# Performance work log

Hardware: AMD Instinct MI355X
Metric: run time of the kernel (lower is better)

## Reference

```python
import jax, jax.numpy as jnp
import numpy as np

E = 1024

def setup_inputs() -> dict:
    key = jax.random.key(0)
    ks = jax.random.split(key, 9)
    s = 1.0 / np.sqrt(E)
    return {
        "x": jax.random.normal(ks[0], (4, 2048, E), dtype=jnp.float32),
        "Wq": jax.random.uniform(ks[1], (E, E), jnp.float32, -s, s),
        "bq": jax.random.uniform(ks[2], (E,), jnp.float32, -s, s),
        "Wk": jax.random.uniform(ks[3], (E, E), jnp.float32, -s, s),
        "bk": jax.random.uniform(ks[4], (E,), jnp.float32, -s, s),
        "Wv": jax.random.uniform(ks[5], (E, E), jnp.float32, -s, s),
        "bv": jax.random.uniform(ks[6], (E,), jnp.float32, -s, s),
        "Wo": jax.random.uniform(ks[7], (E, E), jnp.float32, -s, s),
        "bo": jax.random.uniform(ks[8], (E,), jnp.float32, -s, s),
    }

def reference(x, Wq, bq, Wk, bk, Wv, bv, Wo, bo):
    # Note: the torch module never splits heads; attention is over full embed_dim.
    # nn.Linear: y = x @ W.T + b
    Q = jnp.einsum('bse,fe->bsf', x, Wq) + bq
    K = jnp.einsum('bse,fe->bsf', x, Wk) + bk
    V = jnp.einsum('bse,fe->bsf', x, Wv) + bv
    scale = 1.0 / jnp.sqrt(jnp.asarray(x.shape[-1], x.dtype))
    scores = jnp.einsum('bqe,bke->bqk', Q, K) * scale  # [B, S, S]
    weights = jax.nn.softmax(scores, axis=-1)
    out = jnp.einsum('bqk,bke->bqe', weights, V)
    # dropout is identity in eval mode
    return jnp.einsum('bse,fe->bsf', out, Wo) + bo
```

## Files before the change

kernel.cpp:

```cpp
#include <hip/hip_runtime.h>
#include <hip/hip_bf16.h>
#include <stdint.h>

typedef short bf16x8 __attribute__((ext_vector_type(8)));
typedef float f32x4 __attribute__((ext_vector_type(4)));
typedef __attribute__((address_space(3))) void lds_void_t;
typedef __attribute__((address_space(1))) void g_void_t;

static __device__ __forceinline__ unsigned short f2b(float f) {
    __hip_bfloat16 b = __float2bfloat16(f);
    return __builtin_bit_cast(unsigned short, b);
}
static __device__ __forceinline__ float b2f(unsigned int u) {
    return __builtin_bit_cast(float, u << 16);
}

__global__ __launch_bounds__(256) void cast_f32_bf16(
    const float* __restrict__ in, ushort* __restrict__ out, int n4)
{
    int i = blockIdx.x * blockDim.x + threadIdx.x;
    const int stride = gridDim.x * blockDim.x;
    for (; i < n4; i += stride) {
        float4 v = reinterpret_cast<const float4*>(in)[i];
        ushort4 o;
        o.x = f2b(v.x); o.y = f2b(v.y); o.z = f2b(v.z); o.w = f2b(v.w);
        reinterpret_cast<ushort4*>(out)[i] = o;
    }
}

__global__ __launch_bounds__(256) void concat_bias(
    const float* __restrict__ b0, const float* __restrict__ b1,
    const float* __restrict__ b2, float* __restrict__ out)
{
    const int i = blockIdx.x * blockDim.x + threadIdx.x;
    const int sec = i >> 10, off = i & 1023;
    out[i] = sec == 0 ? b0[off] : (sec == 1 ? b1[off] : b2[off]);
}

template<typename CT, bool HAS_BIAS>
__global__ __launch_bounds__(256, 4)
void gemm_bt(const ushort* __restrict__ A, const ushort* __restrict__ B,
             const float* __restrict__ bias, CT* __restrict__ C,
             int lda, int ldb, int ldc, int K,
             long strideA, long strideB, long strideC, float alpha)
{
    __shared__ __align__(16) ushort sA[128 * 64];
    __shared__ __align__(16) ushort sB[128 * 64];

    const int bz = blockIdx.z;
    A += (size_t)bz * strideA;
    B += (size_t)bz * strideB;
    C += (size_t)bz * strideC;

    const int gx = gridDim.x, gy = gridDim.y;
    const int nwg = gx * gy;
    int bx = blockIdx.x, by = blockIdx.y;
    if ((nwg & 7) == 0) {
        const int flat = blockIdx.x + gx * blockIdx.y;
        const int cpx = nwg >> 3;
        const int u = (flat & 7) * cpx + (flat >> 3);
        bx = u % gx;
        by = u / gx;
    }

    const int tid = threadIdx.x;
    const int w   = tid >> 6;
    const int l   = tid & 63;
    const int wr  = w >> 1;
    const int wc  = w & 1;

    const int bRow = by * 128;
    const int bCol = bx * 128;

    const int lr   = l >> 3;
    const int scol = (((l & 7) ^ lr) << 3);

    f32x4 acc[4][4];
#pragma unroll
    for (int m = 0; m < 4; ++m)
#pragma unroll
        for (int n = 0; n < 4; ++n)
            acc[m][n] = f32x4{0.f, 0.f, 0.f, 0.f};

    for (int k0 = 0; k0 < K; k0 += 64) {
#pragma unroll
        for (int p = 0; p < 4; ++p) {
            const int c   = p * 4 + w;
            const int row = c * 8 + lr;
            const ushort* gA = A + (size_t)(bRow + row) * lda + (k0 + scol);
            const ushort* gB = B + (size_t)(bCol + row) * ldb + (k0 + scol);
            __builtin_amdgcn_global_load_lds((const g_void_t*)gA,
                (lds_void_t*)((char*)sA + c * 1024), 16, 0, 0);
            __builtin_amdgcn_global_load_lds((const g_void_t*)gB,
                (lds_void_t*)((char*)sB + c * 1024), 16, 0, 0);
        }
        __syncthreads();

        bf16x8 af[4][2], bfv[4][2];
#pragma unroll
        for (int m = 0; m < 4; ++m) {
            const int ar = wr * 64 + m * 16 + (l & 15);
#pragma unroll
            for (int ks = 0; ks < 2; ++ks) {
                const int slot = (ks * 4 + (l >> 4)) ^ (ar & 7);
                af[m][ks] = *reinterpret_cast<const bf16x8*>(
                    (const char*)sA + ar * 128 + slot * 16);
            }
        }
#pragma unroll
        for (int n = 0; n < 4; ++n) {
            const int br = wc * 64 + n * 16 + (l & 15);
#pragma unroll
            for (int ks = 0; ks < 2; ++ks) {
                const int slot = (ks * 4 + (l >> 4)) ^ (br & 7);
                bfv[n][ks] = *reinterpret_cast<const bf16x8*>(
                    (const char*)sB + br * 128 + slot * 16);
            }
        }
#pragma unroll
        for (int ks = 0; ks < 2; ++ks)
#pragma unroll
            for (int m = 0; m < 4; ++m)
#pragma unroll
                for (int n = 0; n < 4; ++n)
                    acc[m][n] = __builtin_amdgcn_mfma_f32_16x16x32_bf16(
                        af[m][ks], bfv[n][ks], acc[m][n], 0, 0, 0);
        __syncthreads();
    }

    const int cl = l & 15;
#pragma unroll
    for (int n = 0; n < 4; ++n) {
        const int col = bCol + wc * 64 + n * 16 + cl;
        const float bv = HAS_BIAS ? bias[col] : 0.f;
#pragma unroll
        for (int m = 0; m < 4; ++m) {
#pragma unroll
            for (int r = 0; r < 4; ++r) {
                const int row = bRow + wr * 64 + m * 16 + (l >> 4) * 4 + r;
                const float v = (acc[m][n][r] + bv) * alpha;
                if constexpr (sizeof(CT) == 2)
                    ((ushort*)C)[(size_t)row * ldc + col] = f2b(v);
                else
                    ((float*)C)[(size_t)row * ldc + col] = v;
            }
        }
    }
}

__global__ __launch_bounds__(256) void softmax_rows(ushort* __restrict__ S)
{
    __shared__ float red[8];
    const size_t row = blockIdx.x;
    ushort* p = S + row * 2048;
    const int tid = threadIdx.x;

    uint4 v = reinterpret_cast<uint4*>(p)[tid];
    float f[8];
    const unsigned int* wv = reinterpret_cast<const unsigned int*>(&v);
#pragma unroll
    for (int j = 0; j < 4; ++j) {
        f[2 * j]     = b2f(wv[j] & 0xFFFFu);
        f[2 * j + 1] = b2f(wv[j] >> 16);
    }
    float mx = f[0];
#pragma unroll
    for (int j = 1; j < 8; ++j) mx = fmaxf(mx, f[j]);
#pragma unroll
    for (int s = 1; s < 64; s <<= 1) mx = fmaxf(mx, __shfl_xor(mx, s));
    if ((tid & 63) == 0) red[tid >> 6] = mx;
    __syncthreads();
    mx = fmaxf(fmaxf(red[0], red[1]), fmaxf(red[2], red[3]));

    float sum = 0.f;
#pragma unroll
    for (int j = 0; j < 8; ++j) { f[j] = __expf(f[j] - mx); sum += f[j]; }
#pragma unroll
    for (int s = 1; s < 64; s <<= 1) sum += __shfl_xor(sum, s);
    if ((tid & 63) == 0) red[4 + (tid >> 6)] = sum;
    __syncthreads();
    sum = (red[4] + red[5]) + (red[6] + red[7]);
    const float inv = 1.0f / sum;

    uint4 o;
    unsigned int* wo = reinterpret_cast<unsigned int*>(&o);
#pragma unroll
    for (int j = 0; j < 4; ++j) {
        const unsigned int lo = f2b(f[2 * j] * inv);
        const unsigned int hi = f2b(f[2 * j + 1] * inv);
        wo[j] = lo | (hi << 16);
    }
    reinterpret_cast<uint4*>(p)[tid] = o;
}

__global__ __launch_bounds__(256) void transpose_v(
    const ushort* __restrict__ V, ushort* __restrict__ Vt, int ldv, long strideV)
{
    __shared__ ushort t[64][65];
    const int b  = blockIdx.z;
    const int e0 = blockIdx.x * 64;
    const int s0 = blockIdx.y * 64;
    const int tid = threadIdx.x;
    const int cg = (tid & 15) * 4;
    const int r0 = tid >> 4;

    const ushort* Vb = V + (size_t)b * strideV;
#pragma unroll
    for (int p = 0; p < 4; ++p) {
        const int r = r0 + p * 16;
        ushort4 x = *reinterpret_cast<const ushort4*>(
            Vb + (size_t)(s0 + r) * ldv + e0 + cg);
        t[r][cg + 0] = x.x; t[r][cg + 1] = x.y;
        t[r][cg + 2] = x.z; t[r][cg + 3] = x.w;
    }
    __syncthreads();
    ushort* Vtb = Vt + (size_t)b * 1024 * 2048;
#pragma unroll
    for (int p = 0; p < 4; ++p) {
        const int e = r0 + p * 16;
        ushort4 o;
        o.x = t[cg + 0][e]; o.y = t[cg + 1][e];
        o.z = t[cg + 2][e]; o.w = t[cg + 3][e];
        *reinterpret_cast<ushort4*>(Vtb + (size_t)(e0 + e) * 2048 + s0 + cg) = o;
    }
}

extern "C" void kernel_launch(void* const* d_in, const int* in_sizes, int n_in,
                              void* d_out, int out_size, void* d_ws, size_t ws_size,
                              hipStream_t stream)
{
    const float* x  = (const float*)d_in[0];
    const float* Wq = (const float*)d_in[1];
    const float* bq = (const float*)d_in[2];
    const float* Wk = (const float*)d_in[3];
    const float* bk = (const float*)d_in[4];
    const float* Wv = (const float*)d_in[5];
    const float* bv = (const float*)d_in[6];
    const float* Wo = (const float*)d_in[7];
    const float* bo = (const float*)d_in[8];

    char* ws = (char*)d_ws;
    ushort* xb    = (ushort*)(ws);
    ushort* Wqkvb = (ushort*)(ws + 16777216);
    ushort* Wob   = (ushort*)(ws + 23068672);
    float*  bqkv  = (float*) (ws + 25165824);
    ushort* QKVb  = (ushort*)(ws + 26214400);
    ushort* Vtb   = (ushort*)(ws + 76546048);
    ushort* Sb    = (ushort*)(ws + 93323264);
    ushort* Ob    = (ushort*)(ws + 126877696);

    cast_f32_bf16<<<2048, 256, 0, stream>>>(x,  xb, 2097152);
    cast_f32_bf16<<<1024, 256, 0, stream>>>(Wq, Wqkvb,           262144);
    cast_f32_bf16<<<1024, 256, 0, stream>>>(Wk, Wqkvb + 1048576, 262144);
    cast_f32_bf16<<<1024, 256, 0, stream>>>(Wv, Wqkvb + 2097152, 262144);
    cast_f32_bf16<<<1024, 256, 0, stream>>>(Wo, Wob, 262144);
    concat_bias<<<12, 256, 0, stream>>>(bq, bk, bv, bqkv);

    gemm_bt<ushort, true><<<dim3(24, 64, 1), 256, 0, stream>>>(
        xb, Wqkvb, bqkv, QKVb, 1024, 1024, 3072, 1024, 0, 0, 0, 1.0f);

    transpose_v<<<dim3(16, 32, 4), 256, 0, stream>>>(
        QKVb + 2048, Vtb, 3072, 2048L * 3072);

    gemm_bt<ushort, false><<<dim3(16, 16, 4), 256, 0, stream>>>(
        QKVb, QKVb + 1024, nullptr, Sb, 3072, 3072, 2048, 1024,
        2048L * 3072, 2048L * 3072, 2048L * 2048, 0.03125f);

    softmax_rows<<<8192, 256, 0, stream>>>(Sb);

    gemm_bt<ushort, false><<<dim3(8, 16, 4), 256, 0, stream>>>(
        Sb, Vtb, nullptr, Ob, 2048, 2048, 1024, 2048,
        2048L * 2048, 1024L * 2048, 2048L * 1024, 1.0f);

    gemm_bt<float, true><<<dim3(8, 64, 1), 256, 0, stream>>>(
        Ob, Wob, bo, (float*)d_out, 1024, 1024, 1024, 1024, 0, 0, 0, 1.0f);
}
```

Baseline: 303.5 us.

## Fuse prep casts into one kernel and stage bf16 GEMM epilogue through LDS

Merges the five cast launches and the bias concat into a single prep kernel, cutting launch overhead and gaps between launches. For bf16-output GEMMs, the epilogue now writes the tile to shared memory and then stores 16-byte coalesced rows, replacing scattered 2-byte stores. Wob now aliases Wqkvb+3M, which is the same offset as before. The staged epilogue adds a barrier and LDS traffic.

```diff
diff --git a/kernel.cpp b/kernel.cpp
--- a/kernel.cpp
+++ b/kernel.cpp
@@ -15,26 +15,37 @@
     return __builtin_bit_cast(float, u << 16);
 }
 
-__global__ __launch_bounds__(256) void cast_f32_bf16(
-    const float* __restrict__ in, ushort* __restrict__ out, int n4)
-{
-    int i = blockIdx.x * blockDim.x + threadIdx.x;
-    const int stride = gridDim.x * blockDim.x;
-    for (; i < n4; i += stride) {
-        float4 v = reinterpret_cast<const float4*>(in)[i];
+__global__ __launch_bounds__(256) void prep(
+    const float* __restrict__ x,
+    const float* __restrict__ wq, const float* __restrict__ wk,
+    const float* __restrict__ wv, const float* __restrict__ wo,
+    const float* __restrict__ bq, const float* __restrict__ bk,
+    const float* __restrict__ bv_, float* __restrict__ bqkv,
+    ushort* __restrict__ xb, ushort* __restrict__ wqkvb)
+{
+    const int T = 3145728;
+    int i = blockIdx.x * 256 + threadIdx.x;
+    const int stride = gridDim.x * 256;
+    for (; i < T; i += stride) {
+        const float* src; ushort* dst; int off;
+        if (i < 2097152) { src = x; dst = xb; off = i; }
+        else {
+            const int j = i - 2097152;
+            const int w = j >> 18;
+            off = j & 262143;
+            src = (w == 0) ? wq : (w == 1) ? wk : (w == 2) ? wv : wo;
+            dst = wqkvb + (w << 20);
+        }
+        float4 v = reinterpret_cast<const float4*>(src)[off];
         ushort4 o;
         o.x = f2b(v.x); o.y = f2b(v.y); o.z = f2b(v.z); o.w = f2b(v.w);
-        reinterpret_cast<ushort4*>(out)[i] = o;
-    }
-}
-
-__global__ __launch_bounds__(256) void concat_bias(
-    const float* __restrict__ b0, const float* __restrict__ b1,
-    const float* __restrict__ b2, float* __restrict__ out)
-{
-    const int i = blockIdx.x * blockDim.x + threadIdx.x;
-    const int sec = i >> 10, off = i & 1023;
-    out[i] = sec == 0 ? b0[off] : (sec == 1 ? b1[off] : b2[off]);
+        reinterpret_cast<ushort4*>(dst)[off] = o;
+    }
+    const int t = blockIdx.x * 256 + threadIdx.x;
+    if (t < 3072) {
+        const int sec = t >> 10, of = t & 1023;
+        bqkv[t] = sec == 0 ? bq[of] : (sec == 1 ? bk[of] : bv_[of]);
+    }
 }
 
 template<typename CT, bool HAS_BIAS>
@@ -44,8 +55,9 @@
              int lda, int ldb, int ldc, int K,
              long strideA, long strideB, long strideC, float alpha)
 {
-    __shared__ __align__(16) ushort sA[128 * 64];
-    __shared__ __align__(16) ushort sB[128 * 64];
+    __shared__ __align__(16) ushort smem[128 * 64 * 2];
+    ushort* sA = smem;
+    ushort* sB = smem + 128 * 64;
 
     const int bz = blockIdx.z;
     A += (size_t)bz * strideA;
@@ -129,20 +141,42 @@
     }
 
     const int cl = l & 15;
-#pragma unroll
-    for (int n = 0; n < 4; ++n) {
-        const int col = bCol + wc * 64 + n * 16 + cl;
-        const float bv = HAS_BIAS ? bias[col] : 0.f;
-#pragma unroll
-        for (int m = 0; m < 4; ++m) {
-#pragma unroll
-            for (int r = 0; r < 4; ++r) {
-                const int row = bRow + wr * 64 + m * 16 + (l >> 4) * 4 + r;
-                const float v = (acc[m][n][r] + bv) * alpha;
-                if constexpr (sizeof(CT) == 2)
-                    ((ushort*)C)[(size_t)row * ldc + col] = f2b(v);
-                else
-                    ((float*)C)[(size_t)row * ldc + col] = v;
+    if constexpr (sizeof(CT) == 2) {
+        ushort* st = smem;
+#pragma unroll
+        for (int n = 0; n < 4; ++n) {
+            const int col = wc * 64 + n * 16 + cl;
+            const float bv = HAS_BIAS ? bias[bCol + col] : 0.f;
+#pragma unroll
+            for (int m = 0; m < 4; ++m) {
+                const int row0 = wr * 64 + m * 16 + (l >> 4) * 4;
+#pragma unroll
+                for (int r = 0; r < 4; ++r)
+                    st[(row0 + r) * 128 + col] = f2b((acc[m][n][r] + bv) * alpha);
+            }
+        }
+        __syncthreads();
+#pragma unroll
+        for (int i = 0; i < 8; ++i) {
+            const int c    = tid + i * 256;
+            const int row  = c >> 4;
+            const int col8 = (c & 15) * 8;
+            *reinterpret_cast<uint4*>(
+                (ushort*)C + (size_t)(bRow + row) * ldc + bCol + col8) =
+                *reinterpret_cast<const uint4*>(st + row * 128 + col8);
+        }
+    } else {
+#pragma unroll
+        for (int n = 0; n < 4; ++n) {
+            const int col = bCol + wc * 64 + n * 16 + cl;
+            const float bv = HAS_BIAS ? bias[col] : 0.f;
+#pragma unroll
+            for (int m = 0; m < 4; ++m) {
+#pragma unroll
+                for (int r = 0; r < 4; ++r) {
+                    const int row = bRow + wr * 64 + m * 16 + (l >> 4) * 4 + r;
+                    ((float*)C)[(size_t)row * ldc + col] = (acc[m][n][r] + bv) * alpha;
+                }
             }
         }
     }
@@ -242,19 +276,14 @@
     char* ws = (char*)d_ws;
     ushort* xb    = (ushort*)(ws);
     ushort* Wqkvb = (ushort*)(ws + 16777216);
-    ushort* Wob   = (ushort*)(ws + 23068672);
+    ushort* Wob   = Wqkvb + 3 * 1048576;
     float*  bqkv  = (float*) (ws + 25165824);
     ushort* QKVb  = (ushort*)(ws + 26214400);
     ushort* Vtb   = (ushort*)(ws + 76546048);
     ushort* Sb    = (ushort*)(ws + 93323264);
     ushort* Ob    = (ushort*)(ws + 126877696);
 
-    cast_f32_bf16<<<2048, 256, 0, stream>>>(x,  xb, 2097152);
-    cast_f32_bf16<<<1024, 256, 0, stream>>>(Wq, Wqkvb,           262144);
-    cast_f32_bf16<<<1024, 256, 0, stream>>>(Wk, Wqkvb + 1048576, 262144);
-    cast_f32_bf16<<<1024, 256, 0, stream>>>(Wv, Wqkvb + 2097152, 262144);
-    cast_f32_bf16<<<1024, 256, 0, stream>>>(Wo, Wob, 262144);
-    concat_bias<<<12, 256, 0, stream>>>(bq, bk, bv, bqkv);
+    prep<<<2048, 256, 0, stream>>>(x, Wq, Wk, Wv, Wo, bq, bk, bv, bqkv, xb, Wqkvb);
 
     gemm_bt<ushort, true><<<dim3(24, 64, 1), 256, 0, stream>>>(
         xb, Wqkvb, bqkv, QKVb, 1024, 1024, 3072, 1024, 0, 0, 0, 1.0f);
```

Measured after the change: 293.6 us. 3.3% less time.
